# Performance work log

Measured on AMD Instinct MI355X. Metric: run time of the kernel, lower is better.

Reference implementation:

```python
import jax, jax.numpy as jnp
import numpy as np

SEQ = 2048          # prompt length (x.size(0) > 1 path)
D_IN = 4096         # weight.size(1)
N_OUT = 11008       # weight.size(0), Llama-7B FFN width
SPARSITY = 0.4      # fraction of neurons kept globally
TOKEN_SPARSITY = 0.2  # per-token top-k fraction (common.get_core_neurons)


def setup_inputs() -> dict:
    key = jax.random.key(0)
    kx, kw, kb = jax.random.split(key, 3)
    x = jax.random.normal(kx, (SEQ, D_IN), dtype=jnp.float16)
    weight = jax.random.normal(kw, (N_OUT, D_IN), dtype=jnp.float16) * jnp.float16(0.02)
    bias = jax.random.normal(kb, (N_OUT,), dtype=jnp.float16) * jnp.float16(0.02)
    return {"x": x, "weight": weight, "bias": bias}


def get_core_neurons(true_value, token_sparsity, sparsity, n_neurons):
    # Per-token top-k activations -> count how often each neuron appears ->
    # keep the globally most frequent `sparsity * n_neurons` neurons (sorted).
    k_tok = int(token_sparsity * n_neurons)
    remained = int(sparsity * n_neurons)
    _, tok_idx = jax.lax.top_k(true_value.astype(jnp.float32), k_tok)  # [SEQ, k_tok]
    counts = jnp.zeros((n_neurons,), dtype=jnp.int32).at[tok_idx.reshape(-1)].add(1)
    _, core_idx = jax.lax.top_k(counts, remained)
    return jnp.sort(core_idx)


def reference(x, weight, bias):
    # Prompt path: full GEMM in fp16, then core-neuron selection + weight gather.
    true_value = x @ weight.T + bias                      # [SEQ, N_OUT] fp16
    core_idx = get_core_neurons(true_value, TOKEN_SPARSITY, SPARSITY, weight.shape[0])
    filtered_W = weight[core_idx, :]                      # [remained, D_IN]
    filtered_bias = bias[core_idx]                        # [remained]
    return true_value, filtered_W, filtered_bias
```

## Files before the change

### kernel.cpp

```cpp
#include <hip/hip_runtime.h>

typedef __attribute__((ext_vector_type(8))) _Float16 half8;
typedef __attribute__((ext_vector_type(4))) float floatx4;
typedef unsigned short us_t;

#define SEQ   2048
#define DIN   4096
#define NOUT  11008
#define KTOK  2201
#define NCORE 4403
#define NCHUNK 43
#define NBLK  1376

__device__ __forceinline__ unsigned pk2(float a, float b) {
  auto h = __builtin_amdgcn_cvt_pkrtz(a, b);
  return __builtin_bit_cast(unsigned, h);
}
__device__ __forceinline__ unsigned fkey32(unsigned u) {
  return u ^ ((u >> 31) ? 0xFFFFFFFFu : 0x80000000u);
}
__device__ __forceinline__ void gl2lds16(const us_t* g, us_t* l) {
  __builtin_amdgcn_global_load_lds(
      (const __attribute__((address_space(1))) unsigned int*)(g),
      (__attribute__((address_space(3))) unsigned int*)(l), 16, 0, 0);
}

__global__ __launch_bounds__(256) void cvt_f16(const float* __restrict__ src,
                                               unsigned* __restrict__ dst, int n8) {
  int i = blockIdx.x * 256 + threadIdx.x;
  if (i >= n8) return;
  const float4* s = (const float4*)src + (size_t)i * 2;
  float4 a = s[0], b = s[1];
  uint4 o = {pk2(a.x, a.y), pk2(a.z, a.w), pk2(b.x, b.y), pk2(b.z, b.w)};
  ((uint4*)dst)[i] = o;
}

__global__ __launch_bounds__(256) void gemm_f16(const us_t* __restrict__ X16,
                                                const us_t* __restrict__ W16,
                                                const float* __restrict__ Bias,
                                                float* __restrict__ C) {
  __shared__ __attribute__((aligned(16))) us_t As[128 * 32];
  __shared__ __attribute__((aligned(16))) us_t Bs[128 * 32];
  const int t = threadIdx.x;

  const int id = blockIdx.x;
  const int wg = ((id & 7) * (NBLK / 8)) + (id >> 3);
  const int n0 = (wg >> 4) * 128;
  const int m0 = (wg & 15) * 128;

  const int l = t & 63, w = t >> 6;
  const int r = l & 15, q = l >> 4;
  const int wm = (w >> 1) * 64, wn = (w & 1) * 64;

  const us_t* Ag = X16 + (size_t)(m0 + (t >> 2)) * DIN + (t & 3) * 8;
  const us_t* Bg = W16 + (size_t)(n0 + (t >> 2)) * DIN + (t & 3) * 8;
  us_t* la = As + t * 8;
  us_t* lb = Bs + t * 8;

  floatx4 acc[4][4] = {};
  const us_t* pa = As + (wm + r) * 32 + q * 8;
  const us_t* pb = Bs + (wn + r) * 32 + q * 8;

  for (int kt = 0; kt < DIN; kt += 32) {
    gl2lds16(Ag + kt, la);
    gl2lds16(Ag + kt + 64 * DIN, la + 2048);
    gl2lds16(Bg + kt, lb);
    gl2lds16(Bg + kt + 64 * DIN, lb + 2048);
    __syncthreads();
    half8 af[4];
#pragma unroll
    for (int im = 0; im < 4; ++im)
      af[im] = *(const half8*)(pa + im * 16 * 32);
#pragma unroll
    for (int in = 0; in < 4; ++in) {
      half8 bfv = *(const half8*)(pb + in * 16 * 32);
#pragma unroll
      for (int im = 0; im < 4; ++im)
        acc[im][in] = __builtin_amdgcn_mfma_f32_16x16x32_f16(af[im], bfv, acc[im][in], 0, 0, 0);
    }
    __syncthreads();
  }
#pragma unroll
  for (int in = 0; in < 4; ++in) {
    const int col = n0 + wn + in * 16 + r;
    const float bv = Bias[col];
#pragma unroll
    for (int im = 0; im < 4; ++im) {
      const int row = m0 + wm + im * 16 + q * 4;
#pragma unroll
      for (int i = 0; i < 4; ++i)
        C[(size_t)(row + i) * NOUT + col] = acc[im][in][i] + bv;
    }
  }
}

__global__ __launch_bounds__(256) void gemm_bias(const float* __restrict__ X,
                                                 const float* __restrict__ W,
                                                 const float* __restrict__ Bias,
                                                 float* __restrict__ C) {
  __shared__ __attribute__((aligned(16))) us_t As[128 * 32];
  __shared__ __attribute__((aligned(16))) us_t Bs[128 * 32];
  const int t = threadIdx.x;
  const int m0 = blockIdx.y * 128, n0 = blockIdx.x * 128;
  const int l = t & 63, w = t >> 6;
  const int r = l & 15, q = l >> 4;
  const int wm = (w >> 1) * 64, wn = (w & 1) * 64;
  const float* Ag = X + (size_t)(m0 + (t >> 2)) * DIN + (t & 3) * 8;
  const float* Bg = W + (size_t)(n0 + (t >> 2)) * DIN + (t & 3) * 8;
  us_t* la = As + t * 8;
  us_t* lb = Bs + t * 8;
  floatx4 acc[4][4] = {};
  const us_t* pa = As + (wm + r) * 32 + q * 8;
  const us_t* pb = Bs + (wn + r) * 32 + q * 8;
  for (int kt = 0; kt < DIN; kt += 32) {
    float4 a0 = *(const float4*)(Ag + kt);
    float4 a1 = *(const float4*)(Ag + kt + 4);
    float4 a2 = *(const float4*)(Ag + kt + 64 * DIN);
    float4 a3 = *(const float4*)(Ag + kt + 64 * DIN + 4);
    float4 b0 = *(const float4*)(Bg + kt);
    float4 b1 = *(const float4*)(Bg + kt + 4);
    float4 b2 = *(const float4*)(Bg + kt + 64 * DIN);
    float4 b3 = *(const float4*)(Bg + kt + 64 * DIN + 4);
    uint4 ua  = {pk2(a0.x, a0.y), pk2(a0.z, a0.w), pk2(a1.x, a1.y), pk2(a1.z, a1.w)};
    uint4 ua2 = {pk2(a2.x, a2.y), pk2(a2.z, a2.w), pk2(a3.x, a3.y), pk2(a3.z, a3.w)};
    uint4 ub  = {pk2(b0.x, b0.y), pk2(b0.z, b0.w), pk2(b1.x, b1.y), pk2(b1.z, b1.w)};
    uint4 ub2 = {pk2(b2.x, b2.y), pk2(b2.z, b2.w), pk2(b3.x, b3.y), pk2(b3.z, b3.w)};
    *(uint4*)la = ua;
    *(uint4*)(la + 2048) = ua2;
    *(uint4*)lb = ub;
    *(uint4*)(lb + 2048) = ub2;
    __syncthreads();
    half8 af[4];
#pragma unroll
    for (int im = 0; im < 4; ++im)
      af[im] = *(const half8*)(pa + im * 16 * 32);
#pragma unroll
    for (int in = 0; in < 4; ++in) {
      half8 bfv = *(const half8*)(pb + in * 16 * 32);
#pragma unroll
      for (int im = 0; im < 4; ++im)
        acc[im][in] = __builtin_amdgcn_mfma_f32_16x16x32_f16(af[im], bfv, acc[im][in], 0, 0, 0);
    }
    __syncthreads();
  }
#pragma unroll
  for (int in = 0; in < 4; ++in) {
    const int col = n0 + wn + in * 16 + r;
    const float bv = Bias[col];
#pragma unroll
    for (int im = 0; im < 4; ++im) {
      const int row = m0 + wm + im * 16 + q * 4;
#pragma unroll
      for (int i = 0; i < 4; ++i)
        C[(size_t)(row + i) * NOUT + col] = acc[im][in][i] + bv;
    }
  }
}

__global__ __launch_bounds__(256) void row_topk(const float* __restrict__ TV,
                                                int* __restrict__ counts) {
  __shared__ __attribute__((aligned(16))) unsigned keys[NOUT];
  __shared__ int hist[2048];
  __shared__ int csum[256];
  __shared__ int shv[2];
  __shared__ int cnte[NCHUNK * 4];
  const int t = threadIdx.x;
  const int lane = t & 63, wv = t >> 6;

  for (int i = t; i < 2048; i += 256) hist[i] = 0;
  __syncthreads();
  const uint4* src = (const uint4*)(TV + (size_t)blockIdx.x * NOUT);
  for (int i = t; i < NOUT / 4; i += 256) {
    uint4 v = src[i];
    unsigned k0 = fkey32(v.x), k1 = fkey32(v.y), k2 = fkey32(v.z), k3 = fkey32(v.w);
    uint4 kk = {k0, k1, k2, k3};
    *(uint4*)&keys[i * 4] = kk;
    atomicAdd(&hist[k0 >> 21], 1);
    atomicAdd(&hist[k1 >> 21], 1);
    atomicAdd(&hist[k2 >> 21], 1);
    atomicAdd(&hist[k3 >> 21], 1);
  }
  __syncthreads();
  { int s = 0; for (int j = 0; j < 8; ++j) s += hist[t * 8 + j]; csum[t] = s; }
  __syncthreads();
  if (t == 0) {
    int cum = 0;
    for (int c = 255; c >= 0; --c) {
      if (cum + csum[c] >= KTOK) {
        for (int v = c * 8 + 7; v >= c * 8; --v) {
          if (cum + hist[v] >= KTOK) { shv[0] = v; shv[1] = cum; break; }
          cum += hist[v];
        }
        break;
      }
      cum += csum[c];
    }
  }
  __syncthreads();
  const unsigned b1 = (unsigned)shv[0];
  const int above1 = shv[1];
  __syncthreads();

  for (int i = t; i < 2048; i += 256) hist[i] = 0;
  __syncthreads();
  for (int i = t; i < NOUT; i += 256) {
    unsigned k = keys[i];
    if ((k >> 21) == b1) atomicAdd(&hist[(k >> 10) & 0x7FF], 1);
  }
  __syncthreads();
  { int s = 0; for (int j = 0; j < 8; ++j) s += hist[t * 8 + j]; csum[t] = s; }
  __syncthreads();
  if (t == 0) {
    int cum = above1;
    for (int c = 255; c >= 0; --c) {
      if (cum + csum[c] >= KTOK) {
        for (int v = c * 8 + 7; v >= c * 8; --v) {
          if (cum + hist[v] >= KTOK) { shv[0] = v; shv[1] = cum; break; }
          cum += hist[v];
        }
        break;
      }
      cum += csum[c];
    }
  }
  __syncthreads();
  const unsigned b2 = (unsigned)shv[0];
  const int above2 = shv[1];
  const unsigned pref2 = (b1 << 11) | b2;
  __syncthreads();

  for (int i = t; i < 1024; i += 256) hist[i] = 0;
  __syncthreads();
  for (int i = t; i < NOUT; i += 256) {
    unsigned k = keys[i];
    if ((k >> 10) == pref2) atomicAdd(&hist[k & 0x3FF], 1);
  }
  __syncthreads();
  { int s = 0; if (t < 128) { for (int j = 0; j < 8; ++j) s += hist[t * 8 + j]; } csum[t] = s; }
  __syncthreads();
  if (t == 0) {
    int cum = above2;
    for (int c = 127; c >= 0; --c) {
      if (cum + csum[c] >= KTOK) {
        for (int v = c * 8 + 7; v >= c * 8; --v) {
          if (cum + hist[v] >= KTOK) { shv[0] = v; shv[1] = cum; break; }
          cum += hist[v];
        }
        break;
      }
      cum += csum[c];
    }
  }
  __syncthreads();
  const unsigned T = (pref2 << 10) | (unsigned)shv[0];
  const int need = KTOK - shv[1];

  for (int c = 0; c < NCHUNK; ++c) {
    const int i = c * 256 + t;
    const unsigned k = keys[i];
    if (k > T) atomicAdd(&counts[i], 1);
    unsigned long long me = __ballot(k == T);
    if (lane == 0) cnte[c * 4 + wv] = __popcll(me);
  }
  __syncthreads();
  for (int c = 0; c < NCHUNK; ++c) {
    const int i = c * 256 + t;
    const unsigned k = keys[i];
    const bool eq = (k == T);
    unsigned long long me = __ballot(eq);
    if (eq) {
      int rank = __popcll(me & ((1ULL << lane) - 1));
      const int idx = c * 4 + wv;
      for (int j = 0; j < idx; ++j) rank += cnte[j];
      if (rank < need) atomicAdd(&counts[i], 1);
    }
  }
}

__global__ __launch_bounds__(256) void select_core(const int* __restrict__ counts,
                                                   const float* __restrict__ Bias,
                                                   int* __restrict__ core_idx,
                                                   float* __restrict__ bias_out) {
  __shared__ int cl[NOUT];
  __shared__ int hist[2049];
  __shared__ int csum[257];
  __shared__ int shv[2];
  __shared__ int tabS[256];
  const int t = threadIdx.x;
  const int lane = t & 63, wv = t >> 6;
  for (int i = t; i < NOUT; i += 256) cl[i] = counts[i];
  for (int i = t; i < 2049; i += 256) hist[i] = 0;
  tabS[t] = 0;
  __syncthreads();
  for (int i = t; i < NOUT; i += 256) atomicAdd(&hist[cl[i]], 1);
  __syncthreads();
  { int s = 0; for (int j = 0; j < 8; ++j) s += hist[t * 8 + j]; csum[t] = s;
    if (t == 0) csum[256] = hist[2048]; }
  __syncthreads();
  if (t == 0) {
    int cum = 0;
    for (int c = 256; c >= 0; --c) {
      if (cum + csum[c] >= NCORE) {
        int hi = (c == 256) ? 2048 : c * 8 + 7;
        for (int v = hi; v >= c * 8; --v) {
          if (cum + hist[v] >= NCORE) { shv[0] = v; shv[1] = NCORE - cum; break; }
          cum += hist[v];
        }
        break;
      }
      cum += csum[c];
    }
  }
  __syncthreads();
  const int Cv = shv[0], need2 = shv[1];
  for (int c = 0; c < NCHUNK; ++c) {
    const int i = c * 256 + t;
    const int cnt = cl[i];
    unsigned long long mg = __ballot(cnt > Cv);
    unsigned long long me = __ballot(cnt == Cv);
    if (lane == 0) tabS[c * 4 + wv] = __popcll(mg) | (__popcll(me) << 16);
  }
  __syncthreads();
  int orig = tabS[t];
  for (int off = 1; off < 256; off <<= 1) {
    int v = (t >= off) ? tabS[t - off] : 0;
    __syncthreads();
    tabS[t] += v;
    __syncthreads();
  }
  int excl = tabS[t] - orig;
  __syncthreads();
  tabS[t] = excl;
  __syncthreads();
  const unsigned long long lm = (1ULL << lane) - 1;
  for (int c = 0; c < NCHUNK; ++c) {
    const int i = c * 256 + t;
    const int cnt = cl[i];
    const bool g = cnt > Cv, e = cnt == Cv;
    unsigned long long mg = __ballot(g);
    unsigned long long me = __ballot(e);
    const int P = tabS[c * 4 + wv];
    const int gpre = (P & 0xFFFF) + __popcll(mg & lm);
    const int epre = (P >> 16) + __popcll(me & lm);
    const bool sel = g || (e && epre < need2);
    if (sel) {
      const int pos = gpre + (epre < need2 ? epre : need2);
      core_idx[pos] = i;
      bias_out[pos] = Bias[i];
    }
  }
}

__global__ __launch_bounds__(256) void gather_rows(const float* __restrict__ W,
                                                   const int* __restrict__ core_idx,
                                                   float* __restrict__ outW) {
  const int b = blockIdx.x;
  const int j = core_idx[b];
  const float4* src = (const float4*)(W + (size_t)j * DIN);
  float4* dst = (float4*)(outW + (size_t)b * DIN);
  for (int i = threadIdx.x; i < DIN / 4; i += 256) dst[i] = src[i];
}

__global__ __launch_bounds__(256) void zero_counts(int* __restrict__ counts) {
  counts[blockIdx.x * 256 + threadIdx.x] = 0;
}

extern "C" void kernel_launch(void* const* d_in, const int* in_sizes, int n_in,
                              void* d_out, int out_size, void* d_ws, size_t ws_size,
                              hipStream_t stream) {
  const float* X    = (const float*)d_in[0];
  const float* W    = (const float*)d_in[1];
  const float* Bias = (const float*)d_in[2];
  float* out_tv = (float*)d_out;
  float* out_w  = out_tv + (size_t)SEQ * NOUT;
  float* out_b  = out_w + (size_t)NCORE * DIN;
  int* counts   = (int*)d_ws;
  int* core_idx = counts + NOUT;

  const size_t meta = 64 * 1024;
  const size_t need_ws = meta + ((size_t)SEQ * DIN + (size_t)NOUT * DIN) * sizeof(us_t);

  zero_counts<<<NOUT / 256, 256, 0, stream>>>(counts);
  if (ws_size >= need_ws) {
    us_t* X16 = (us_t*)((char*)d_ws + meta);
    us_t* W16 = X16 + (size_t)SEQ * DIN;
    cvt_f16<<<(SEQ * DIN / 8 + 255) / 256, 256, 0, stream>>>(X, (unsigned*)X16, SEQ * DIN / 8);
    cvt_f16<<<(NOUT * DIN / 8 + 255) / 256, 256, 0, stream>>>(W, (unsigned*)W16, NOUT * DIN / 8);
    gemm_f16<<<NBLK, 256, 0, stream>>>(X16, W16, Bias, out_tv);
  } else {
    gemm_bias<<<dim3(NOUT / 128, SEQ / 128), 256, 0, stream>>>(X, W, Bias, out_tv);
  }
  row_topk<<<SEQ, 256, 0, stream>>>(out_tv, counts);
  select_core<<<1, 256, 0, stream>>>(counts, Bias, core_idx, out_b);
  gather_rows<<<NCORE, 256, 0, stream>>>(W, core_idx, out_w);
}
```

Before: 749.4 us.

## Double-buffer GEMM with swizzled 64-wide K tiles and parallel-scan radix select

The fp16 GEMM now uses double-buffered LDS tiles of K=64 with an XOR swizzle, so the next tile's global-to-LDS loads overlap the MFMAs on the current tile. Explicit vmcnt waits and setprio are used around the compute. Separately, the top-k radix select replaces the single-thread serial bucket scans with a 256-thread suffix scan in LDS plus a parallel boundary search. This cuts serial per-token latency but adds more barriers, and the larger LDS footprint may lower occupancy.

```diff
diff --git a/kernel.cpp b/kernel.cpp
--- a/kernel.cpp
+++ b/kernel.cpp
@@ -39,8 +39,8 @@
                                                 const us_t* __restrict__ W16,
                                                 const float* __restrict__ Bias,
                                                 float* __restrict__ C) {
-  __shared__ __attribute__((aligned(16))) us_t As[128 * 32];
-  __shared__ __attribute__((aligned(16))) us_t Bs[128 * 32];
+  __shared__ __attribute__((aligned(16))) us_t As[2][128 * 64];
+  __shared__ __attribute__((aligned(16))) us_t Bs[2][128 * 64];
   const int t = threadIdx.x;
 
   const int id = blockIdx.x;
@@ -49,37 +49,79 @@
   const int m0 = (wg & 15) * 128;
 
   const int l = t & 63, w = t >> 6;
-  const int r = l & 15, q = l >> 4;
+  const int r = l & 15, q = l >> 4, sw = l & 7;
   const int wm = (w >> 1) * 64, wn = (w & 1) * 64;
 
-  const us_t* Ag = X16 + (size_t)(m0 + (t >> 2)) * DIN + (t & 3) * 8;
-  const us_t* Bg = W16 + (size_t)(n0 + (t >> 2)) * DIN + (t & 3) * 8;
-  us_t* la = As + t * 8;
-  us_t* lb = Bs + t * 8;
+  const int tr = t >> 3;
+  const int csw = ((t & 7) ^ (tr & 7)) * 8;
+  const us_t* Ag = X16 + (size_t)(m0 + tr) * DIN + csw;
+  const us_t* Bg = W16 + (size_t)(n0 + tr) * DIN + csw;
 
   floatx4 acc[4][4] = {};
-  const us_t* pa = As + (wm + r) * 32 + q * 8;
-  const us_t* pb = Bs + (wn + r) * 32 + q * 8;
-
-  for (int kt = 0; kt < DIN; kt += 32) {
-    gl2lds16(Ag + kt, la);
-    gl2lds16(Ag + kt + 64 * DIN, la + 2048);
-    gl2lds16(Bg + kt, lb);
-    gl2lds16(Bg + kt + 64 * DIN, lb + 2048);
-    __syncthreads();
-    half8 af[4];
-#pragma unroll
-    for (int im = 0; im < 4; ++im)
-      af[im] = *(const half8*)(pa + im * 16 * 32);
+
+  const int s0 = (q ^ sw) * 8;
+  const int s1 = ((4 + q) ^ sw) * 8;
+  const int ra = (wm + r) * 64;
+  const int rb = (wn + r) * 64;
+
+#define STAGE8(bb, kt)                                                   \
+  {                                                                      \
+    const us_t* a_ = Ag + (kt);                                          \
+    const us_t* b_ = Bg + (kt);                                          \
+    us_t* la_ = &As[bb][t * 8];                                          \
+    us_t* lb_ = &Bs[bb][t * 8];                                          \
+    gl2lds16(a_, la_);                                                   \
+    gl2lds16(a_ + 32 * DIN, la_ + 2048);                                 \
+    gl2lds16(a_ + 64 * DIN, la_ + 4096);                                 \
+    gl2lds16(a_ + 96 * DIN, la_ + 6144);                                 \
+    gl2lds16(b_, lb_);                                                   \
+    gl2lds16(b_ + 32 * DIN, lb_ + 2048);                                 \
+    gl2lds16(b_ + 64 * DIN, lb_ + 4096);                                 \
+    gl2lds16(b_ + 96 * DIN, lb_ + 6144);                                 \
+  }
+
+  STAGE8(0, 0);
+  int buf = 0;
+  for (int kt = 0; kt < DIN; kt += 64, buf ^= 1) {
+    if (kt + 64 < DIN) {
+      STAGE8(buf ^ 1, kt + 64);
+      asm volatile("s_waitcnt vmcnt(8)" ::: "memory");
+    } else {
+      asm volatile("s_waitcnt vmcnt(0)" ::: "memory");
+    }
+    __builtin_amdgcn_s_barrier();
+    __builtin_amdgcn_sched_barrier(0);
+
+    const us_t* Ab = &As[buf][0];
+    const us_t* Bb = &Bs[buf][0];
+    half8 a0[4], a1[4], b0[4], b1[4];
+#pragma unroll
+    for (int im = 0; im < 4; ++im) {
+      a0[im] = *(const half8*)(Ab + ra + im * 1024 + s0);
+      a1[im] = *(const half8*)(Ab + ra + im * 1024 + s1);
+    }
 #pragma unroll
     for (int in = 0; in < 4; ++in) {
-      half8 bfv = *(const half8*)(pb + in * 16 * 32);
+      b0[in] = *(const half8*)(Bb + rb + in * 1024 + s0);
+      b1[in] = *(const half8*)(Bb + rb + in * 1024 + s1);
+    }
+    __builtin_amdgcn_s_setprio(1);
+#pragma unroll
+    for (int in = 0; in < 4; ++in)
 #pragma unroll
       for (int im = 0; im < 4; ++im)
-        acc[im][in] = __builtin_amdgcn_mfma_f32_16x16x32_f16(af[im], bfv, acc[im][in], 0, 0, 0);
-    }
-    __syncthreads();
-  }
+        acc[im][in] = __builtin_amdgcn_mfma_f32_16x16x32_f16(a0[im], b0[in], acc[im][in], 0, 0, 0);
+#pragma unroll
+    for (int in = 0; in < 4; ++in)
+#pragma unroll
+      for (int im = 0; im < 4; ++im)
+        acc[im][in] = __builtin_amdgcn_mfma_f32_16x16x32_f16(a1[im], b1[in], acc[im][in], 0, 0, 0);
+    __builtin_amdgcn_s_setprio(0);
+    __builtin_amdgcn_sched_barrier(0);
+    __builtin_amdgcn_s_barrier();
+  }
+#undef STAGE8
+
 #pragma unroll
   for (int in = 0; in < 4; ++in) {
     const int col = n0 + wn + in * 16 + r;
@@ -183,17 +225,21 @@
   __syncthreads();
   { int s = 0; for (int j = 0; j < 8; ++j) s += hist[t * 8 + j]; csum[t] = s; }
   __syncthreads();
-  if (t == 0) {
-    int cum = 0;
-    for (int c = 255; c >= 0; --c) {
-      if (cum + csum[c] >= KTOK) {
-        for (int v = c * 8 + 7; v >= c * 8; --v) {
-          if (cum + hist[v] >= KTOK) { shv[0] = v; shv[1] = cum; break; }
-          cum += hist[v];
-        }
-        break;
+  for (int off = 1; off < 256; off <<= 1) {
+    int u = (t + off < 256) ? csum[t + off] : 0;
+    __syncthreads();
+    csum[t] += u;
+    __syncthreads();
+  }
+  {
+    const bool c0 = csum[t] >= KTOK;
+    const bool c1 = (t < 255) && (csum[t + 1] >= KTOK);
+    if (c0 && !c1) {
+      int cum = (t < 255) ? csum[t + 1] : 0;
+      for (int v = t * 8 + 7; v >= t * 8; --v) {
+        if (cum + hist[v] >= KTOK) { shv[0] = v; shv[1] = cum; break; }
+        cum += hist[v];
       }
-      cum += csum[c];
     }
   }
   __syncthreads();
@@ -210,17 +256,21 @@
   __syncthreads();
   { int s = 0; for (int j = 0; j < 8; ++j) s += hist[t * 8 + j]; csum[t] = s; }
   __syncthreads();
-  if (t == 0) {
-    int cum = above1;
-    for (int c = 255; c >= 0; --c) {
-      if (cum + csum[c] >= KTOK) {
-        for (int v = c * 8 + 7; v >= c * 8; --v) {
-          if (cum + hist[v] >= KTOK) { shv[0] = v; shv[1] = cum; break; }
-          cum += hist[v];
-        }
-        break;
+  for (int off = 1; off < 256; off <<= 1) {
+    int u = (t + off < 256) ? csum[t + off] : 0;
+    __syncthreads();
+    csum[t] += u;
+    __syncthreads();
+  }
+  {
+    const bool c0 = above1 + csum[t] >= KTOK;
+    const bool c1 = (t < 255) && (above1 + csum[t + 1] >= KTOK);
+    if (c0 && !c1) {
+      int cum = above1 + ((t < 255) ? csum[t + 1] : 0);
+      for (int v = t * 8 + 7; v >= t * 8; --v) {
+        if (cum + hist[v] >= KTOK) { shv[0] = v; shv[1] = cum; break; }
+        cum += hist[v];
       }
-      cum += csum[c];
     }
   }
   __syncthreads();
@@ -238,17 +288,21 @@
   __syncthreads();
   { int s = 0; if (t < 128) { for (int j = 0; j < 8; ++j) s += hist[t * 8 + j]; } csum[t] = s; }
   __syncthreads();
-  if (t == 0) {
-    int cum = above2;
-    for (int c = 127; c >= 0; --c) {
-      if (cum + csum[c] >= KTOK) {
-        for (int v = c * 8 + 7; v >= c * 8; --v) {
-          if (cum + hist[v] >= KTOK) { shv[0] = v; shv[1] = cum; break; }
-          cum += hist[v];
-        }
-        break;
+  for (int off = 1; off < 256; off <<= 1) {
+    int u = (t + off < 256) ? csum[t + off] : 0;
+    __syncthreads();
+    csum[t] += u;
+    __syncthreads();
+  }
+  {
+    const bool c0 = above2 + csum[t] >= KTOK;
+    const bool c1 = (t < 255) && (above2 + csum[t + 1] >= KTOK);
+    if (c0 && !c1) {
+      int cum = above2 + ((t < 255) ? csum[t + 1] : 0);
+      for (int v = t * 8 + 7; v >= t * 8; --v) {
+        if (cum + hist[v] >= KTOK) { shv[0] = v; shv[1] = cum; break; }
+        cum += hist[v];
       }
-      cum += csum[c];
     }
   }
   __syncthreads();
```

Result: no change. 747.8 us (-0.2%).

## Parallelize threshold scans, widen row_topk blocks, gather rows from fp16 weights

Applied to the files above, without the earlier changes.

Replaces the single-thread serial histogram threshold scans in row_topk and select_core with wave-shuffle suffix scans, where each thread checks whether its histogram bucket group crosses the threshold. row_topk now runs with 512 threads per block. select_core's LDS Hillis-Steele prefix scan becomes a shuffle-based scan. The gather now reads the fp16 weight copy and widens it to fp32, halving the read bytes. Fp16 inputs make that round trip exact.

```diff
diff --git a/kernel.cpp b/kernel.cpp
--- a/kernel.cpp
+++ b/kernel.cpp
@@ -10,6 +10,8 @@
 #define KTOK  2201
 #define NCORE 4403
 #define NCHUNK 43
+#define NT2   512
+#define NCH2  22
 #define NBLK  1376
 
 __device__ __forceinline__ unsigned pk2(float a, float b) {
@@ -23,6 +25,40 @@
   __builtin_amdgcn_global_load_lds(
       (const __attribute__((address_space(1))) unsigned int*)(g),
       (__attribute__((address_space(3))) unsigned int*)(l), 16, 0, 0);
+}
+
+__device__ __forceinline__ int wave_suffix_incl(int x, int lane) {
+#pragma unroll
+  for (int off = 1; off < 64; off <<= 1) {
+    int y = __shfl_down(x, off);
+    x += (lane + off < 64) ? y : 0;
+  }
+  return x;
+}
+
+template <int G, int NW>
+__device__ __forceinline__ void find_thr(const int* hist, int above, int K,
+                                         int* wtot, int* shv,
+                                         int t, int lane, int wv) {
+  int val = 0;
+#pragma unroll
+  for (int j = 0; j < G; ++j) val += hist[t * G + j];
+  int x = wave_suffix_incl(val, lane);
+  if (lane == 0) wtot[wv] = x;
+  __syncthreads();
+  int add = 0;
+#pragma unroll
+  for (int w2 = 0; w2 < NW; ++w2) add += (w2 > wv) ? wtot[w2] : 0;
+  const int suf = x + add;
+  const int sufn = suf - val;
+  if (above + suf >= K && above + sufn < K) {
+    int cum = above + sufn;
+    for (int v = t * G + G - 1; v >= t * G; --v) {
+      if (cum + hist[v] >= K) { shv[0] = v; shv[1] = cum; break; }
+      cum += hist[v];
+    }
+  }
+  __syncthreads();
 }
 
 __global__ __launch_bounds__(256) void cvt_f16(const float* __restrict__ src,
@@ -157,20 +193,20 @@
   }
 }
 
-__global__ __launch_bounds__(256) void row_topk(const float* __restrict__ TV,
+__global__ __launch_bounds__(NT2) void row_topk(const float* __restrict__ TV,
                                                 int* __restrict__ counts) {
   __shared__ __attribute__((aligned(16))) unsigned keys[NOUT];
   __shared__ int hist[2048];
-  __shared__ int csum[256];
+  __shared__ int wtot[NT2 / 64];
   __shared__ int shv[2];
-  __shared__ int cnte[NCHUNK * 4];
+  __shared__ int cnte[NCH2 * (NT2 / 64)];
   const int t = threadIdx.x;
   const int lane = t & 63, wv = t >> 6;
 
-  for (int i = t; i < 2048; i += 256) hist[i] = 0;
+  for (int i = t; i < 2048; i += NT2) hist[i] = 0;
   __syncthreads();
   const uint4* src = (const uint4*)(TV + (size_t)blockIdx.x * NOUT);
-  for (int i = t; i < NOUT / 4; i += 256) {
+  for (int i = t; i < NOUT / 4; i += NT2) {
     uint4 v = src[i];
     unsigned k0 = fkey32(v.x), k1 = fkey32(v.y), k2 = fkey32(v.z), k3 = fkey32(v.w);
     uint4 kk = {k0, k1, k2, k3};
@@ -181,96 +217,53 @@
     atomicAdd(&hist[k3 >> 21], 1);
   }
   __syncthreads();
-  { int s = 0; for (int j = 0; j < 8; ++j) s += hist[t * 8 + j]; csum[t] = s; }
-  __syncthreads();
-  if (t == 0) {
-    int cum = 0;
-    for (int c = 255; c >= 0; --c) {
-      if (cum + csum[c] >= KTOK) {
-        for (int v = c * 8 + 7; v >= c * 8; --v) {
-          if (cum + hist[v] >= KTOK) { shv[0] = v; shv[1] = cum; break; }
-          cum += hist[v];
-        }
-        break;
-      }
-      cum += csum[c];
-    }
-  }
-  __syncthreads();
+  find_thr<4, NT2 / 64>(hist, 0, KTOK, wtot, shv, t, lane, wv);
   const unsigned b1 = (unsigned)shv[0];
   const int above1 = shv[1];
   __syncthreads();
 
-  for (int i = t; i < 2048; i += 256) hist[i] = 0;
-  __syncthreads();
-  for (int i = t; i < NOUT; i += 256) {
+  for (int i = t; i < 2048; i += NT2) hist[i] = 0;
+  __syncthreads();
+  for (int i = t; i < NOUT; i += NT2) {
     unsigned k = keys[i];
     if ((k >> 21) == b1) atomicAdd(&hist[(k >> 10) & 0x7FF], 1);
   }
   __syncthreads();
-  { int s = 0; for (int j = 0; j < 8; ++j) s += hist[t * 8 + j]; csum[t] = s; }
-  __syncthreads();
-  if (t == 0) {
-    int cum = above1;
-    for (int c = 255; c >= 0; --c) {
-      if (cum + csum[c] >= KTOK) {
-        for (int v = c * 8 + 7; v >= c * 8; --v) {
-          if (cum + hist[v] >= KTOK) { shv[0] = v; shv[1] = cum; break; }
-          cum += hist[v];
-        }
-        break;
-      }
-      cum += csum[c];
-    }
-  }
-  __syncthreads();
+  find_thr<4, NT2 / 64>(hist, above1, KTOK, wtot, shv, t, lane, wv);
   const unsigned b2 = (unsigned)shv[0];
   const int above2 = shv[1];
   const unsigned pref2 = (b1 << 11) | b2;
   __syncthreads();
 
-  for (int i = t; i < 1024; i += 256) hist[i] = 0;
-  __syncthreads();
-  for (int i = t; i < NOUT; i += 256) {
+  for (int i = t; i < 1024; i += NT2) hist[i] = 0;
+  __syncthreads();
+  for (int i = t; i < NOUT; i += NT2) {
     unsigned k = keys[i];
     if ((k >> 10) == pref2) atomicAdd(&hist[k & 0x3FF], 1);
   }
   __syncthreads();
-  { int s = 0; if (t < 128) { for (int j = 0; j < 8; ++j) s += hist[t * 8 + j]; } csum[t] = s; }
-  __syncthreads();
-  if (t == 0) {
-    int cum = above2;
-    for (int c = 127; c >= 0; --c) {
-      if (cum + csum[c] >= KTOK) {
-        for (int v = c * 8 + 7; v >= c * 8; --v) {
-          if (cum + hist[v] >= KTOK) { shv[0] = v; shv[1] = cum; break; }
-          cum += hist[v];
-        }
-        break;
-      }
-      cum += csum[c];
-    }
-  }
-  __syncthreads();
+  find_thr<2, NT2 / 64>(hist, above2, KTOK, wtot, shv, t, lane, wv);
   const unsigned T = (pref2 << 10) | (unsigned)shv[0];
   const int need = KTOK - shv[1];
 
-  for (int c = 0; c < NCHUNK; ++c) {
-    const int i = c * 256 + t;
-    const unsigned k = keys[i];
-    if (k > T) atomicAdd(&counts[i], 1);
-    unsigned long long me = __ballot(k == T);
-    if (lane == 0) cnte[c * 4 + wv] = __popcll(me);
-  }
-  __syncthreads();
-  for (int c = 0; c < NCHUNK; ++c) {
-    const int i = c * 256 + t;
-    const unsigned k = keys[i];
-    const bool eq = (k == T);
+  for (int c = 0; c < NCH2; ++c) {
+    const int i = c * NT2 + t;
+    const bool valid = i < NOUT;
+    const unsigned k = valid ? keys[i] : 0u;
+    if (valid && k > T) atomicAdd(&counts[i], 1);
+    unsigned long long me = __ballot(valid && (k == T));
+    if (lane == 0) cnte[c * (NT2 / 64) + wv] = __popcll(me);
+  }
+  __syncthreads();
+  for (int c = 0; c < NCH2; ++c) {
+    const int i = c * NT2 + t;
+    const bool valid = i < NOUT;
+    const unsigned k = valid ? keys[i] : 0u;
+    const bool eq = valid && (k == T);
     unsigned long long me = __ballot(eq);
     if (eq) {
       int rank = __popcll(me & ((1ULL << lane) - 1));
-      const int idx = c * 4 + wv;
+      const int idx = c * (NT2 / 64) + wv;
       for (int j = 0; j < idx; ++j) rank += cnte[j];
       if (rank < need) atomicAdd(&counts[i], 1);
     }
@@ -283,35 +276,39 @@
                                                    float* __restrict__ bias_out) {
   __shared__ int cl[NOUT];
   __shared__ int hist[2049];
-  __shared__ int csum[257];
+  __shared__ int wtot[4];
   __shared__ int shv[2];
   __shared__ int tabS[256];
   const int t = threadIdx.x;
   const int lane = t & 63, wv = t >> 6;
   for (int i = t; i < NOUT; i += 256) cl[i] = counts[i];
   for (int i = t; i < 2049; i += 256) hist[i] = 0;
-  tabS[t] = 0;
   __syncthreads();
   for (int i = t; i < NOUT; i += 256) atomicAdd(&hist[cl[i]], 1);
   __syncthreads();
-  { int s = 0; for (int j = 0; j < 8; ++j) s += hist[t * 8 + j]; csum[t] = s;
-    if (t == 0) csum[256] = hist[2048]; }
-  __syncthreads();
-  if (t == 0) {
-    int cum = 0;
-    for (int c = 256; c >= 0; --c) {
-      if (cum + csum[c] >= NCORE) {
-        int hi = (c == 256) ? 2048 : c * 8 + 7;
-        for (int v = hi; v >= c * 8; --v) {
-          if (cum + hist[v] >= NCORE) { shv[0] = v; shv[1] = NCORE - cum; break; }
-          cum += hist[v];
-        }
-        break;
+  {
+    int val = 0;
+#pragma unroll
+    for (int j = 0; j < 8; ++j) val += hist[t * 8 + j];
+    if (t == 255) val += hist[2048];
+    int x = wave_suffix_incl(val, lane);
+    if (lane == 0) wtot[wv] = x;
+    __syncthreads();
+    int add = 0;
+#pragma unroll
+    for (int w2 = 0; w2 < 4; ++w2) add += (w2 > wv) ? wtot[w2] : 0;
+    const int suf = x + add;
+    const int sufn = suf - val;
+    if (suf >= NCORE && sufn < NCORE) {
+      int cum = sufn;
+      const int hi = (t == 255) ? 2048 : t * 8 + 7;
+      for (int v = hi; v >= t * 8; --v) {
+        if (cum + hist[v] >= NCORE) { shv[0] = v; shv[1] = NCORE - cum; break; }
+        cum += hist[v];
       }
-      cum += csum[c];
-    }
-  }
-  __syncthreads();
+    }
+    __syncthreads();
+  }
   const int Cv = shv[0], need2 = shv[1];
   for (int c = 0; c < NCHUNK; ++c) {
     const int i = c * 256 + t;
@@ -319,19 +316,28 @@
     unsigned long long mg = __ballot(cnt > Cv);
     unsigned long long me = __ballot(cnt == Cv);
     if (lane == 0) tabS[c * 4 + wv] = __popcll(mg) | (__popcll(me) << 16);
-  }
-  __syncthreads();
-  int orig = tabS[t];
-  for (int off = 1; off < 256; off <<= 1) {
-    int v = (t >= off) ? tabS[t - off] : 0;
-    __syncthreads();
-    tabS[t] += v;
-    __syncthreads();
-  }
-  int excl = tabS[t] - orig;
-  __syncthreads();
-  tabS[t] = excl;
-  __syncthreads();
+    else if (c == 0) tabS[c * 4 + wv] = tabS[c * 4 + wv];
+  }
+  if (t >= NCHUNK * 4) tabS[t] = 0;
+  __syncthreads();
+  {
+    const int orig = tabS[t];
+    int x = orig;
+#pragma unroll
+    for (int off = 1; off < 64; off <<= 1) {
+      int y = __shfl_up(x, off);
+      x += (lane >= off) ? y : 0;
+    }
+    if (lane == 63) wtot[wv] = x;
+    __syncthreads();
+    int add = 0;
+#pragma unroll
+    for (int w2 = 0; w2 < 4; ++w2) add += (w2 < wv) ? wtot[w2] : 0;
+    const int excl = x - orig + add;
+    __syncthreads();
+    tabS[t] = excl;
+    __syncthreads();
+  }
   const unsigned long long lm = (1ULL << lane) - 1;
   for (int c = 0; c < NCHUNK; ++c) {
     const int i = c * 256 + t;
@@ -351,6 +357,22 @@
   }
 }
 
+__global__ __launch_bounds__(256) void gather_rows16(const us_t* __restrict__ W16,
+                                                     const int* __restrict__ core_idx,
+                                                     float* __restrict__ outW) {
+  const int b = blockIdx.x;
+  const int j = core_idx[b];
+  const half8* src = (const half8*)(W16 + (size_t)j * DIN);
+  float4* dst = (float4*)(outW + (size_t)b * DIN);
+  for (int i = threadIdx.x; i < DIN / 8; i += 256) {
+    half8 h = src[i];
+    float4 lo = {(float)h[0], (float)h[1], (float)h[2], (float)h[3]};
+    float4 hi = {(float)h[4], (float)h[5], (float)h[6], (float)h[7]};
+    dst[i * 2] = lo;
+    dst[i * 2 + 1] = hi;
+  }
+}
+
 __global__ __launch_bounds__(256) void gather_rows(const float* __restrict__ W,
                                                    const int* __restrict__ core_idx,
                                                    float* __restrict__ outW) {
@@ -387,10 +409,13 @@
     cvt_f16<<<(SEQ * DIN / 8 + 255) / 256, 256, 0, stream>>>(X, (unsigned*)X16, SEQ * DIN / 8);
     cvt_f16<<<(NOUT * DIN / 8 + 255) / 256, 256, 0, stream>>>(W, (unsigned*)W16, NOUT * DIN / 8);
     gemm_f16<<<NBLK, 256, 0, stream>>>(X16, W16, Bias, out_tv);
+    row_topk<<<SEQ, NT2, 0, stream>>>(out_tv, counts);
+    select_core<<<1, 256, 0, stream>>>(counts, Bias, core_idx, out_b);
+    gather_rows16<<<NCORE, 256, 0, stream>>>(W16, core_idx, out_w);
   } else {
     gemm_bias<<<dim3(NOUT / 128, SEQ / 128), 256, 0, stream>>>(X, W, Bias, out_tv);
-  }
-  row_topk<<<SEQ, 256, 0, stream>>>(out_tv, counts);
-  select_core<<<1, 256, 0, stream>>>(counts, Bias, core_idx, out_b);
-  gather_rows<<<NCORE, 256, 0, stream>>>(W, core_idx, out_w);
-}
+    row_topk<<<SEQ, NT2, 0, stream>>>(out_tv, counts);
+    select_core<<<1, 256, 0, stream>>>(counts, Bias, core_idx, out_b);
+    gather_rows<<<NCORE, 256, 0, stream>>>(W, core_idx, out_w);
+  }
+}
```

New measurement: 681.7 us. -9.0%, faster.
